# Kernel optimization log

Measured on AMD Instinct MI355X. Metric: run time of the kernel, lower is better.

## Reference

```python
import jax, jax.numpy as jnp
import numpy as np

NUM_HEADS = 8
D_MODEL = 512
D_K = D_MODEL // NUM_HEADS


def setup_inputs() -> dict:
    key = jax.random.key(0)
    ks = jax.random.split(key, 16)
    B, L, Dq = 4, 2048, 512
    s = 1.0 / np.sqrt(D_MODEL)
    inp = {
        "query": jax.random.normal(ks[0], (B, L, Dq), jnp.float32),
        "key": jax.random.normal(ks[1], (B, L, Dq), jnp.float32),
        "value": jax.random.normal(ks[2], (B, L, Dq), jnp.float32),
        "mask": jax.random.randint(ks[3], (B, L), 0, 2, jnp.int32),
        "Wq": jax.random.normal(ks[4], (Dq, D_MODEL), jnp.float32) * s,
        "bq": jax.random.normal(ks[5], (D_MODEL,), jnp.float32) * s,
        "Wk": jax.random.normal(ks[6], (Dq, D_MODEL), jnp.float32) * s,
        "bk": jax.random.normal(ks[7], (D_MODEL,), jnp.float32) * s,
        "Wv": jax.random.normal(ks[8], (Dq, D_MODEL), jnp.float32) * s,
        "bv": jax.random.normal(ks[9], (D_MODEL,), jnp.float32) * s,
        "Wo": jax.random.normal(ks[10], (D_MODEL, D_MODEL), jnp.float32) * s,
        "bo": jax.random.normal(ks[11], (D_MODEL,), jnp.float32) * s,
    }
    return inp


def _mha(query, key, value, mask, Wq, bq, Wk, bk, Wv, bv, Wo, bo):
    B, Q, _ = query.shape
    KV = key.shape[1]
    # projections, split into heads: (B, H, L, d_k)
    q = (query @ Wq + bq).reshape(B, Q, NUM_HEADS, D_K).transpose(0, 2, 1, 3)
    k = (key @ Wk + bk).reshape(B, KV, NUM_HEADS, D_K).transpose(0, 2, 1, 3)
    v = (value @ Wv + bv).reshape(B, KV, NUM_HEADS, D_K).transpose(0, 2, 1, 3)
    # full (B, H, Q, KV) score matrix, as in the original module
    scores = jnp.einsum("bhqd,bhkd->bhqk", q, k) / jnp.sqrt(jnp.asarray(D_K, q.dtype))
    m = (mask == 0)[:, None, None, :]  # (B,1,1,KV) broadcasting like unsqueeze(1)
    min_val = jnp.finfo(scores.dtype).min
    scores = jnp.where(m, min_val, scores)
    attn = jax.nn.softmax(scores, axis=-1)
    attn = jnp.where(m, 0.0, attn)
    xs = jnp.einsum("bhqk,bhkd->bhqd", attn, v)
    xs = xs.transpose(0, 2, 1, 3).reshape(B, Q, NUM_HEADS * D_K)
    return xs @ Wo + bo


def reference(query, key, value, mask, Wq, bq, Wk, bk, Wv, bv, Wo, bo):
    return _mha(query, key, value, mask, Wq, bq, Wk, bk, Wv, bv, Wo, bo)
```

## Files before the change

### kernel.cpp

```cpp
#include <hip/hip_runtime.h>
#include <math.h>

#define Bq 4
#define Lq 2048
#define NH 8
#define LDP6 36

typedef __attribute__((ext_vector_type(8))) __bf16 bf16x8;
typedef __attribute__((ext_vector_type(4))) float f32x4;
#define MFMA16(a,b,c) __builtin_amdgcn_mfma_f32_16x16x32_bf16(a,b,c,0,0,0)

__device__ __forceinline__ void async16(const void* g, void* l) {
    __builtin_amdgcn_global_load_lds(
        (const __attribute__((address_space(1))) unsigned int*)g,
        (__attribute__((address_space(3))) unsigned int*)l, 16, 0, 0);
}

__device__ __forceinline__ void splitbf(float x, ushort& h, ushort& l) {
    unsigned u = __float_as_uint(x);
    h = (ushort)(u >> 16);
    float hf = __uint_as_float(u & 0xffff0000u);
    l = (ushort)(__float_as_uint(x - hf) >> 16);
}
__device__ __forceinline__ ushort rnebf(float x) {
    unsigned u = __float_as_uint(x);
    return (ushort)((u + 0x7fffu + ((u >> 16) & 1u)) >> 16);
}

__global__ __launch_bounds__(256) void prep_kernel(
    const float* __restrict__ W0, const float* __restrict__ W1,
    const float* __restrict__ W2, const float* __restrict__ W3,
    ushort* __restrict__ WTh, ushort* __restrict__ WTl,
    const int* __restrict__ mask, int* __restrict__ idx, int* __restrict__ nvalid)
{
    const int tid = threadIdx.x;
    if (blockIdx.z == 4) {
        if (blockIdx.x >= 4 || blockIdx.y != 0) return;
        __shared__ int ss[256];
        const int b = blockIdx.x;
        int m[8], s = 0;
        #pragma unroll
        for (int j = 0; j < 8; ++j) { m[j] = (mask[b * 2048 + tid * 8 + j] != 0); s += m[j]; }
        int v = s;
        ss[tid] = v;
        __syncthreads();
        for (int off = 1; off < 256; off <<= 1) {
            int t_ = (tid >= off) ? ss[tid - off] : 0;
            __syncthreads();
            v += t_;
            ss[tid] = v;
            __syncthreads();
        }
        int pos = v - s;
        #pragma unroll
        for (int j = 0; j < 8; ++j) if (m[j]) idx[b * 2048 + pos++] = tid * 8 + j;
        int tot = ss[255];
        if (tid == 0) nvalid[b] = tot;
        for (int k = tot + tid; k < 2048; k += 256) idx[b * 2048 + k] = 0;
        return;
    }
    __shared__ float T[64][65];
    const int z = blockIdx.z;
    const float* W = (z == 0) ? W0 : (z == 1) ? W1 : (z == 2) ? W2 : W3;
    const int k0 = blockIdx.x * 64, n0 = blockIdx.y * 64;
    #pragma unroll
    for (int i = 0; i < 4; ++i) {
        int u = tid + i * 256;
        int row = u >> 4, c4 = (u & 15) * 4;
        float4 v = *(const float4*)(W + (size_t)(k0 + row) * 512 + n0 + c4);
        T[row][c4 + 0] = v.x; T[row][c4 + 1] = v.y; T[row][c4 + 2] = v.z; T[row][c4 + 3] = v.w;
    }
    __syncthreads();
    #pragma unroll
    for (int i = 0; i < 2; ++i) {
        int u = tid + i * 256;
        int d = u >> 3, c8 = (u & 7) * 8;
        ushort hs[8], ls[8];
        #pragma unroll
        for (int j = 0; j < 8; ++j) splitbf(T[c8 + j][d], hs[j], ls[j]);
        uint4 wh, wl;
        wh.x = hs[0] | ((unsigned)hs[1] << 16); wh.y = hs[2] | ((unsigned)hs[3] << 16);
        wh.z = hs[4] | ((unsigned)hs[5] << 16); wh.w = hs[6] | ((unsigned)hs[7] << 16);
        wl.x = ls[0] | ((unsigned)ls[1] << 16); wl.y = ls[2] | ((unsigned)ls[3] << 16);
        wl.z = ls[4] | ((unsigned)ls[5] << 16); wl.w = ls[6] | ((unsigned)ls[7] << 16);
        size_t off = (size_t)(z * 512 + n0 + d) * 512 + k0 + c8;
        *(uint4*)(WTh + off) = wh;
        *(uint4*)(WTl + off) = wl;
    }
}

union GS {
    struct {
        ushort A[2][4096];
        ushort Bh[2][4096];
        ushort Bl[2][4096];
    } s;
    ushort E[24576];
};

__global__ __launch_bounds__(256) void gemmqkv_kernel(
    const float* __restrict__ Xq, const float* __restrict__ Xk, const float* __restrict__ Xv,
    const int* __restrict__ idx, const int* __restrict__ nvalid,
    const ushort* __restrict__ BhT, const ushort* __restrict__ BlT,
    const float* __restrict__ b0, const float* __restrict__ b1, const float* __restrict__ b2,
    ushort* __restrict__ Qh, ushort* __restrict__ Khp, ushort* __restrict__ VhT)
{
    __shared__ __align__(16) GS gs;
    const int tid = threadIdx.x;
    const int wave = tid >> 6, lane = tid & 63;
    const int l15 = lane & 15, quad = lane >> 4;
    const int m0 = blockIdx.x * 128;
    const int yy = blockIdx.y;
    const int mi = yy >> 2, n0 = (yy & 3) * 128;
    const int nglob = mi * 512 + n0;
    const int b = m0 >> 11;

    if (mi >= 1) {
        int nv = nvalid[b];
        int nvpad = ((nv + 127) >> 7) << 7;
        if ((m0 & 2047) >= nvpad) return;
    }

    const float* X = (mi == 0) ? Xq : (mi == 1) ? Xk : Xv;
    const float* bias = (mi == 0) ? b0 : (mi == 1) ? b1 : b2;
    const int wm = (wave & 1) * 64, wn = (wave >> 1) * 64;

    const int am = tid >> 3, ak = (tid & 7) * 4;
    const float* asrc[4]; int adst[4];
    #pragma unroll
    for (int i = 0; i < 4; ++i) {
        int row = am + 32 * i;
        int grow = m0 + row, r = grow & 2047;
        int srow = (mi == 0) ? grow : (b * 2048 + idx[b * 2048 + r]);
        asrc[i] = X + (size_t)srow * 512 + ak;
        int c = (tid & 7) >> 1;
        int cp = c ^ ((row >> 1) & 3);
        adst[i] = row * 32 + cp * 8 + (tid & 1) * 4;
    }
    const int brow = lane >> 2;
    const int bcs = ((lane & 3) ^ (brow & 3)) * 8;
    const ushort* bsh[2]; const ushort* bsl[2]; int bdst[2];
    #pragma unroll
    for (int j = 0; j < 2; ++j) {
        int r2 = wave * 32 + j * 16 + brow;
        bsh[j] = BhT + (size_t)(nglob + r2) * 512 + bcs;
        bsl[j] = BlT + (size_t)(nglob + r2) * 512 + bcs;
        bdst[j] = wave * 1024 + j * 512 + lane * 8;
    }

    f32x4 acc[4][4];
    #pragma unroll
    for (int i = 0; i < 4; ++i)
        #pragma unroll
        for (int j = 0; j < 4; ++j) acc[i][j] = (f32x4){0.f, 0.f, 0.f, 0.f};

    float4 av[4];
    #pragma unroll
    for (int i = 0; i < 4; ++i) av[i] = *(const float4*)(asrc[i]);
    #pragma unroll
    for (int j = 0; j < 2; ++j) {
        async16(bsh[j], &gs.s.Bh[0][bdst[j]]);
        async16(bsl[j], &gs.s.Bl[0][bdst[j]]);
    }
    #pragma unroll
    for (int i = 0; i < 4; ++i) {
        ushort4 h4;
        h4.x = rnebf(av[i].x); h4.y = rnebf(av[i].y);
        h4.z = rnebf(av[i].z); h4.w = rnebf(av[i].w);
        *(ushort4*)&gs.s.A[0][adst[i]] = h4;
    }

    for (int t = 0; t < 16; ++t) {
        const int p = t & 1;
        __syncthreads();
        if (t < 15) {
            const int kn = (t + 1) * 32;
            #pragma unroll
            for (int j = 0; j < 2; ++j) {
                async16(bsh[j] + kn, &gs.s.Bh[1 - p][bdst[j]]);
                async16(bsl[j] + kn, &gs.s.Bl[1 - p][bdst[j]]);
            }
            #pragma unroll
            for (int i = 0; i < 4; ++i) av[i] = *(const float4*)(asrc[i] + kn);
        }
        bf16x8 af[4];
        #pragma unroll
        for (int ms = 0; ms < 4; ++ms) {
            int off = (wm + ms * 16 + l15) * 32 + (quad ^ ((l15 >> 1) & 3)) * 8;
            af[ms] = *(const bf16x8*)&gs.s.A[p][off];
        }
        #pragma unroll
        for (int ns = 0; ns < 4; ++ns) {
            int off = (wn + ns * 16 + l15) * 32 + (quad ^ (l15 & 3)) * 8;
            bf16x8 bfh = *(const bf16x8*)&gs.s.Bh[p][off];
            bf16x8 bfl = *(const bf16x8*)&gs.s.Bl[p][off];
            #pragma unroll
            for (int ms = 0; ms < 4; ++ms) {
                acc[ms][ns] = MFMA16(af[ms], bfl, acc[ms][ns]);
                acc[ms][ns] = MFMA16(af[ms], bfh, acc[ms][ns]);
            }
        }
        if (t < 15) {
            #pragma unroll
            for (int i = 0; i < 4; ++i) {
                ushort4 h4;
                h4.x = rnebf(av[i].x); h4.y = rnebf(av[i].y);
                h4.z = rnebf(av[i].z); h4.w = rnebf(av[i].w);
                *(ushort4*)&gs.s.A[1 - p][adst[i]] = h4;
            }
        }
    }

    #pragma unroll
    for (int ns = 0; ns < 4; ++ns) {
        float bv = bias[n0 + wn + ns * 16 + l15];
        #pragma unroll
        for (int ms = 0; ms < 4; ++ms)
            #pragma unroll
            for (int r = 0; r < 4; ++r) acc[ms][ns][r] += bv;
    }

    const int h0 = n0 >> 6;
    const int rr0 = m0 & 2047;
    __syncthreads();
    #pragma unroll
    for (int ms = 0; ms < 4; ++ms) {
        #pragma unroll
        for (int ns = 0; ns < 4; ++ns) {
            int cl = wn + ns * 16 + l15;
            int rl = wm + ms * 16 + quad * 4;
            if (mi == 2) {
                ushort4 w4;
                #pragma unroll
                for (int r = 0; r < 4; ++r) ((ushort*)&w4)[r] = rnebf(acc[ms][ns][r]);
                *(ushort4*)&gs.E[cl * 136 + rl] = w4;
            } else {
                #pragma unroll
                for (int r = 0; r < 4; ++r) gs.E[(rl + r) * 136 + cl] = rnebf(acc[ms][ns][r]);
            }
        }
    }
    __syncthreads();
    if (mi == 2) {
        #pragma unroll
        for (int i = 0; i < 8; ++i) {
            int idx2 = tid + i * 256;
            int d = idx2 >> 4, rg = idx2 & 15;
            int head = d >> 6, dd = d & 63;
            uint4 u = *(const uint4*)&gs.E[d * 136 + rg * 8];
            *(uint4*)&VhT[((size_t)(b * 8 + h0 + head) * 64 + dd) * 2048 + rr0 + rg * 8] = u;
        }
    } else {
        ushort* dst = (mi == 0) ? Qh : Khp;
        #pragma unroll
        for (int i = 0; i < 8; ++i) {
            int idx2 = tid + i * 256;
            int row = idx2 >> 4, cg = idx2 & 15;
            int head = cg >> 3, c8 = (cg & 7) * 8;
            uint4 u = *(const uint4*)&gs.E[row * 136 + cg * 8];
            *(uint4*)&dst[((size_t)(b * 8 + h0 + head) * 2048 + rr0 + row) * 64 + c8] = u;
        }
    }
}

__global__ __launch_bounds__(256) void gemmo_kernel(
    const ushort* __restrict__ Ap,
    const ushort* __restrict__ BhT, const ushort* __restrict__ BlT,
    const float* __restrict__ bias, float* __restrict__ Cf)
{
    __shared__ __align__(16) GS gs;
    const int tid = threadIdx.x;
    const int wave = tid >> 6, lane = tid & 63;
    const int l15 = lane & 15, quad = lane >> 4;
    const int m0 = blockIdx.x * 128;
    const int n0 = blockIdx.y * 128;
    const int wm = (wave & 1) * 64, wn = (wave >> 1) * 64;

    const int arow = lane >> 2;
    const int acs = ((lane & 3) ^ ((arow >> 1) & 3)) * 8;
    const ushort* asrc[2]; int adst[2];
    #pragma unroll
    for (int j = 0; j < 2; ++j) {
        int rb = wave * 2 + j;
        asrc[j] = Ap + (size_t)(m0 + rb * 16 + arow) * 512 + acs;
        adst[j] = rb * 512 + lane * 8;
    }
    const int brow = lane >> 2;
    const int bcs = ((lane & 3) ^ (brow & 3)) * 8;
    const ushort* bsh[2]; const ushort* bsl[2]; int bdst[2];
    #pragma unroll
    for (int j = 0; j < 2; ++j) {
        int r2 = wave * 32 + j * 16 + brow;
        bsh[j] = BhT + (size_t)(n0 + r2) * 512 + bcs;
        bsl[j] = BlT + (size_t)(n0 + r2) * 512 + bcs;
        bdst[j] = wave * 1024 + j * 512 + lane * 8;
    }

    f32x4 acc[4][4];
    #pragma unroll
    for (int i = 0; i < 4; ++i)
        #pragma unroll
        for (int j = 0; j < 4; ++j) acc[i][j] = (f32x4){0.f, 0.f, 0.f, 0.f};

    #pragma unroll
    for (int j = 0; j < 2; ++j) {
        async16(asrc[j], &gs.s.A[0][adst[j]]);
        async16(bsh[j], &gs.s.Bh[0][bdst[j]]);
        async16(bsl[j], &gs.s.Bl[0][bdst[j]]);
    }

    for (int t = 0; t < 16; ++t) {
        const int p = t & 1;
        __syncthreads();
        if (t < 15) {
            const int kn = (t + 1) * 32;
            #pragma unroll
            for (int j = 0; j < 2; ++j) {
                async16(asrc[j] + kn, &gs.s.A[1 - p][adst[j]]);
                async16(bsh[j] + kn, &gs.s.Bh[1 - p][bdst[j]]);
                async16(bsl[j] + kn, &gs.s.Bl[1 - p][bdst[j]]);
            }
        }
        bf16x8 af[4];
        #pragma unroll
        for (int ms = 0; ms < 4; ++ms) {
            int off = (wm + ms * 16 + l15) * 32 + (quad ^ ((l15 >> 1) & 3)) * 8;
            af[ms] = *(const bf16x8*)&gs.s.A[p][off];
        }
        #pragma unroll
        for (int ns = 0; ns < 4; ++ns) {
            int off = (wn + ns * 16 + l15) * 32 + (quad ^ (l15 & 3)) * 8;
            bf16x8 bfh = *(const bf16x8*)&gs.s.Bh[p][off];
            bf16x8 bfl = *(const bf16x8*)&gs.s.Bl[p][off];
            #pragma unroll
            for (int ms = 0; ms < 4; ++ms) {
                acc[ms][ns] = MFMA16(af[ms], bfl, acc[ms][ns]);
                acc[ms][ns] = MFMA16(af[ms], bfh, acc[ms][ns]);
            }
        }
    }

    #pragma unroll
    for (int ns = 0; ns < 4; ++ns) {
        float bv = bias[n0 + wn + ns * 16 + l15];
        #pragma unroll
        for (int ms = 0; ms < 4; ++ms) {
            int col = n0 + wn + ns * 16 + l15;
            #pragma unroll
            for (int r = 0; r < 4; ++r)
                Cf[(size_t)(m0 + wm + ms * 16 + quad * 4 + r) * 512 + col] = acc[ms][ns][r] + bv;
        }
    }
}

union SmemU {
    struct { ushort KVs[2][4][4096]; ushort Pp[8][64 * LDP6]; } p1;
    struct { float Obuf[4][64 * 68]; float Lbuf[4][64]; } p2;
};

__global__ __launch_bounds__(512, 2) void attn3_kernel(
    const ushort* __restrict__ Qh, const ushort* __restrict__ Kh,
    const ushort* __restrict__ VhT, const int* __restrict__ nvalid,
    ushort* __restrict__ XS)
{
    __shared__ SmemU smem;
    const int tid = threadIdx.x;
    const int wave = tid >> 6, lane = tid & 63;
    const int l15 = lane & 15, quad = lane >> 4;
    const int w4 = wave & 3, half = wave >> 2;
    const int bh = blockIdx.x, b = bh >> 3, h = bh & 7;
    const int q0 = blockIdx.y * 256;

    const int nv = nvalid[b];
    const int nt = (nv + 127) >> 7;
    const int kvofs = half * 64 * nt;

    bf16x8 qf[4][2];
    #pragma unroll
    for (int qs = 0; qs < 4; ++qs) {
        size_t qb = ((size_t)bh * 2048 + q0 + w4 * 64 + qs * 16 + l15) * 64 + quad * 8;
        qf[qs][0] = *(const bf16x8*)(Qh + qb);
        qf[qs][1] = *(const bf16x8*)(Qh + qb + 32);
    }

    const f32x4 z = {0.f, 0.f, 0.f, 0.f};
    f32x4 oacc[4][4];
    #pragma unroll
    for (int i = 0; i < 4; ++i)
        #pragma unroll
        for (int j = 0; j < 4; ++j) oacc[i][j] = z;
    float lacc[4] = {0.f, 0.f, 0.f, 0.f};

    const int rloc = lane >> 3, gsw = (lane & 7) ^ rloc;
    const ushort* sb[4]; size_t sstep[4]; int dofs[4];
    #pragma unroll
    for (int i = 0; i < 4; ++i) {
        int cc = wave * 4 + i;
        int hc = cc >> 4, r16 = cc & 15, pc = r16 >> 3, ic = r16 & 7;
        if (pc == 0) {
            sb[i] = Kh + ((size_t)(bh * 2048 + hc * 64 * nt + ic * 8 + rloc)) * 64 + gsw * 8;
            sstep[i] = (size_t)64 * 64;
        } else {
            sb[i] = VhT + ((size_t)(bh * 64 + ic * 8 + rloc)) * 2048 + hc * 64 * nt + gsw * 8;
            sstep[i] = 64;
        }
        dofs[i] = (hc * 2 + pc) * 4096 + ic * 512;
    }

    const int sw0 = (quad ^ (l15 & 7)) * 8;
    const float SCL = 0.18033688011112042f;

    if (nt > 0) {
        #pragma unroll
        for (int i = 0; i < 4; ++i)
            async16(sb[i], &smem.p1.KVs[0][0][0] + dofs[i]);
    }

    for (int t = 0; t < nt; ++t) {
        __syncthreads();
        if (t + 1 < nt) {
            #pragma unroll
            for (int i = 0; i < 4; ++i)
                async16(sb[i] + (size_t)(t + 1) * sstep[i], &smem.p1.KVs[(t + 1) & 1][0][0] + dofs[i]);
        }
        const int p = t & 1;
        const ushort* K0 = smem.p1.KVs[p][half * 2 + 0];
        const ushort* V0 = smem.p1.KVs[p][half * 2 + 1];
        ushort* Pw = smem.p1.Pp[wave];

        #pragma unroll
        for (int ks = 0; ks < 2; ++ks) {
            #pragma unroll
            for (int kt2 = 0; kt2 < 2; ++kt2) {
                const int kt = ks * 2 + kt2;
                const int kb = (kt * 16 + l15) * 64;
                bf16x8 ka0 = *(const bf16x8*)&K0[kb + sw0];
                bf16x8 ka1 = *(const bf16x8*)&K0[kb + (sw0 ^ 32)];
                const int kbase = kvofs + t * 64 + kt * 16 + quad * 4;
                float bias[4];
                #pragma unroll
                for (int r = 0; r < 4; ++r) bias[r] = (kbase + r < nv) ? 0.f : -1e38f;
                #pragma unroll
                for (int qs = 0; qs < 4; ++qs) {
                    f32x4 a = z;
                    a = MFMA16(ka0, qf[qs][0], a);
                    a = MFMA16(ka1, qf[qs][1], a);
                    float pv[4];
                    #pragma unroll
                    for (int r = 0; r < 4; ++r) {
                        float x = __builtin_fmaf(a[r], SCL, bias[r]);
                        float e; asm("v_exp_f32 %0, %1" : "=v"(e) : "v"(x));
                        lacc[qs] += e;
                        pv[r] = e;
                    }
                    unsigned u01, u23;
                    asm("v_cvt_pk_bf16_f32 %0, %1, %2" : "=v"(u01) : "v"(pv[0]), "v"(pv[1]));
                    asm("v_cvt_pk_bf16_f32 %0, %1, %2" : "=v"(u23) : "v"(pv[2]), "v"(pv[3]));
                    uint2 w2; w2.x = u01; w2.y = u23;
                    *(uint2*)&Pw[(qs * 16 + l15) * LDP6 + kt2 * 16 + quad * 4] = w2;
                }
            }
            const int svo = sw0 ^ (ks * 32);
            bf16x8 pf[4];
            #pragma unroll
            for (int qs = 0; qs < 4; ++qs)
                pf[qs] = *(const bf16x8*)&Pw[(qs * 16 + l15) * LDP6 + quad * 8];
            #pragma unroll
            for (int dsub = 0; dsub < 4; ++dsub) {
                const int vb = (dsub * 16 + l15) * 64;
                bf16x8 vh = *(const bf16x8*)&V0[vb + svo];
                #pragma unroll
                for (int qs = 0; qs < 4; ++qs)
                    oacc[qs][dsub] = MFMA16(vh, pf[qs], oacc[qs][dsub]);
            }
        }
    }

    float lv[4];
    #pragma unroll
    for (int qs = 0; qs < 4; ++qs) {
        float v = lacc[qs];
        v += __shfl_xor(v, 16);
        v += __shfl_xor(v, 32);
        lv[qs] = v;
    }

    __syncthreads();
    if (half == 1) {
        #pragma unroll
        for (int qs = 0; qs < 4; ++qs) {
            #pragma unroll
            for (int dsub = 0; dsub < 4; ++dsub) {
                float4 o4 = {oacc[qs][dsub][0], oacc[qs][dsub][1], oacc[qs][dsub][2], oacc[qs][dsub][3]};
                *(float4*)&smem.p2.Obuf[w4][(qs * 16 + l15) * 68 + dsub * 16 + quad * 4] = o4;
            }
            if (quad == 0) smem.p2.Lbuf[w4][qs * 16 + l15] = lv[qs];
        }
    }
    __syncthreads();
    if (half == 0) {
        #pragma unroll
        for (int qs = 0; qs < 4; ++qs) {
            float ltot = lv[qs] + smem.p2.Lbuf[w4][qs * 16 + l15];
            float inv = (ltot > 0.f) ? 1.f / ltot : 0.f;
            int row = q0 + w4 * 64 + qs * 16 + l15;
            ushort* rp = XS + ((size_t)(b * 2048 + row)) * 512 + h * 64;
            #pragma unroll
            for (int dsub = 0; dsub < 4; ++dsub) {
                float4 p4 = *(const float4*)&smem.p2.Obuf[w4][(qs * 16 + l15) * 68 + dsub * 16 + quad * 4];
                ushort4 hv;
                hv.x = rnebf((oacc[qs][dsub][0] + p4.x) * inv);
                hv.y = rnebf((oacc[qs][dsub][1] + p4.y) * inv);
                hv.z = rnebf((oacc[qs][dsub][2] + p4.z) * inv);
                hv.w = rnebf((oacc[qs][dsub][3] + p4.w) * inv);
                *(ushort4*)&rp[dsub * 16 + quad * 4] = hv;
            }
        }
    }
}

extern "C" void kernel_launch(void* const* d_in, const int* in_sizes, int n_in,
                              void* d_out, int out_size, void* d_ws, size_t ws_size,
                              hipStream_t stream) {
    const float* query = (const float*)d_in[0];
    const float* key   = (const float*)d_in[1];
    const float* value = (const float*)d_in[2];
    const int*   mask  = (const int*)d_in[3];
    const float* Wq = (const float*)d_in[4];
    const float* bq = (const float*)d_in[5];
    const float* Wk = (const float*)d_in[6];
    const float* bk = (const float*)d_in[7];
    const float* Wv = (const float*)d_in[8];
    const float* bv = (const float*)d_in[9];
    const float* Wo = (const float*)d_in[10];
    const float* bo = (const float*)d_in[11];

    char* w = (char*)d_ws;
    const size_t MB = (size_t)1 << 20;
    ushort* Qh  = (ushort*)(w + 0 * MB);
    ushort* XS  = (ushort*)(w + 8 * MB);
    ushort* Khp = (ushort*)(w + 16 * MB);
    ushort* VhT = (ushort*)(w + 24 * MB);
    ushort* WTh = (ushort*)(w + 32 * MB);
    ushort* WTl = (ushort*)(w + 34 * MB);
    int* idxbuf = (int*)(w + 36 * MB);
    int* nvbuf  = (int*)(w + 36 * MB + 65536);

    prep_kernel<<<dim3(8, 8, 5), 256, 0, stream>>>(
        Wq, Wk, Wv, Wo, WTh, WTl, mask, idxbuf, nvbuf);
    gemmqkv_kernel<<<dim3(64, 12), 256, 0, stream>>>(
        query, key, value, idxbuf, nvbuf, WTh, WTl, bq, bk, bv, Qh, Khp, VhT);
    attn3_kernel<<<dim3(32, 8), 512, 0, stream>>>(Qh, Khp, VhT, nvbuf, XS);
    gemmo_kernel<<<dim3(64, 4), 256, 0, stream>>>(
        XS, WTh + (size_t)1536 * 512, WTl + (size_t)1536 * 512, bo, (float*)d_out);
}
```

Baseline: 208.1 us.

## Pre-convert QKV inputs to bf16 and drop low-part weight MFMA

The prep kernel now also converts query/key/value from fp32 to bf16 into a workspace buffer. The QKV GEMM can then load A tiles with async global-to-LDS copies instead of register loads plus in-loop rounding. The QKV GEMM also drops the low-order bf16 weight correction term, halving its MFMA count and B-tile traffic. The cost is an extra full pass over the inputs in prep, lower accuracy from single-bf16 weights, and a grid with many early-exit blocks.

```diff
diff --git a/kernel.cpp b/kernel.cpp
--- a/kernel.cpp
+++ b/kernel.cpp
@@ -31,13 +31,62 @@
     const float* __restrict__ W0, const float* __restrict__ W1,
     const float* __restrict__ W2, const float* __restrict__ W3,
     ushort* __restrict__ WTh, ushort* __restrict__ WTl,
-    const int* __restrict__ mask, int* __restrict__ idx, int* __restrict__ nvalid)
+    const int* __restrict__ mask, int* __restrict__ idx, int* __restrict__ nvalid,
+    const float* __restrict__ X0, const float* __restrict__ X1, const float* __restrict__ X2,
+    ushort* __restrict__ Xr)
 {
     const int tid = threadIdx.x;
-    if (blockIdx.z == 4) {
-        if (blockIdx.x >= 4 || blockIdx.y != 0) return;
-        __shared__ int ss[256];
-        const int b = blockIdx.x;
+    const int z = blockIdx.z;
+    if (z < 3) {
+        const float* X = (z == 0) ? X0 : (z == 1) ? X1 : X2;
+        const size_t ebase = (size_t)blockIdx.x * 2048 + (size_t)tid * 8;
+        float4 a = *(const float4*)(X + ebase);
+        float4 bb = *(const float4*)(X + ebase + 4);
+        float vv[8] = {a.x, a.y, a.z, a.w, bb.x, bb.y, bb.z, bb.w};
+        ushort hs[8];
+        #pragma unroll
+        for (int j = 0; j < 8; ++j) hs[j] = rnebf(vv[j]);
+        uint4 wh;
+        wh.x = hs[0] | ((unsigned)hs[1] << 16); wh.y = hs[2] | ((unsigned)hs[3] << 16);
+        wh.z = hs[4] | ((unsigned)hs[5] << 16); wh.w = hs[6] | ((unsigned)hs[7] << 16);
+        *(uint4*)(Xr + (size_t)z * 8192 * 512 + ebase) = wh;
+        return;
+    }
+    const int x = blockIdx.x;
+    __shared__ float T[64][65];
+    __shared__ int ss[256];
+    if (x < 256) {
+        const int m = x >> 6;
+        const float* W = (m == 0) ? W0 : (m == 1) ? W1 : (m == 2) ? W2 : W3;
+        const int k0 = ((x >> 3) & 7) * 64, n0 = (x & 7) * 64;
+        #pragma unroll
+        for (int i = 0; i < 4; ++i) {
+            int u = tid + i * 256;
+            int row = u >> 4, c4 = (u & 15) * 4;
+            float4 v = *(const float4*)(W + (size_t)(k0 + row) * 512 + n0 + c4);
+            T[row][c4 + 0] = v.x; T[row][c4 + 1] = v.y; T[row][c4 + 2] = v.z; T[row][c4 + 3] = v.w;
+        }
+        __syncthreads();
+        #pragma unroll
+        for (int i = 0; i < 2; ++i) {
+            int u = tid + i * 256;
+            int d = u >> 3, c8 = (u & 7) * 8;
+            ushort hs[8], ls[8];
+            #pragma unroll
+            for (int j = 0; j < 8; ++j) splitbf(T[c8 + j][d], hs[j], ls[j]);
+            uint4 wh, wl;
+            wh.x = hs[0] | ((unsigned)hs[1] << 16); wh.y = hs[2] | ((unsigned)hs[3] << 16);
+            wh.z = hs[4] | ((unsigned)hs[5] << 16); wh.w = hs[6] | ((unsigned)hs[7] << 16);
+            wl.x = ls[0] | ((unsigned)ls[1] << 16); wl.y = ls[2] | ((unsigned)ls[3] << 16);
+            wl.z = ls[4] | ((unsigned)ls[5] << 16); wl.w = ls[6] | ((unsigned)ls[7] << 16);
+            size_t off = (size_t)(m * 512 + n0 + d) * 512 + k0 + c8;
+            *(uint4*)(WTh + off) = wh;
+            *(uint4*)(WTl + off) = wl;
+        }
+        return;
+    }
+    if (x < 260) {
+        const int b = x - 256;
         int m[8], s = 0;
         #pragma unroll
         for (int j = 0; j < 8; ++j) { m[j] = (mask[b * 2048 + tid * 8 + j] != 0); s += m[j]; }
@@ -57,51 +106,21 @@
         int tot = ss[255];
         if (tid == 0) nvalid[b] = tot;
         for (int k = tot + tid; k < 2048; k += 256) idx[b * 2048 + k] = 0;
-        return;
-    }
-    __shared__ float T[64][65];
-    const int z = blockIdx.z;
-    const float* W = (z == 0) ? W0 : (z == 1) ? W1 : (z == 2) ? W2 : W3;
-    const int k0 = blockIdx.x * 64, n0 = blockIdx.y * 64;
-    #pragma unroll
-    for (int i = 0; i < 4; ++i) {
-        int u = tid + i * 256;
-        int row = u >> 4, c4 = (u & 15) * 4;
-        float4 v = *(const float4*)(W + (size_t)(k0 + row) * 512 + n0 + c4);
-        T[row][c4 + 0] = v.x; T[row][c4 + 1] = v.y; T[row][c4 + 2] = v.z; T[row][c4 + 3] = v.w;
-    }
-    __syncthreads();
-    #pragma unroll
-    for (int i = 0; i < 2; ++i) {
-        int u = tid + i * 256;
-        int d = u >> 3, c8 = (u & 7) * 8;
-        ushort hs[8], ls[8];
-        #pragma unroll
-        for (int j = 0; j < 8; ++j) splitbf(T[c8 + j][d], hs[j], ls[j]);
-        uint4 wh, wl;
-        wh.x = hs[0] | ((unsigned)hs[1] << 16); wh.y = hs[2] | ((unsigned)hs[3] << 16);
-        wh.z = hs[4] | ((unsigned)hs[5] << 16); wh.w = hs[6] | ((unsigned)hs[7] << 16);
-        wl.x = ls[0] | ((unsigned)ls[1] << 16); wl.y = ls[2] | ((unsigned)ls[3] << 16);
-        wl.z = ls[4] | ((unsigned)ls[5] << 16); wl.w = ls[6] | ((unsigned)ls[7] << 16);
-        size_t off = (size_t)(z * 512 + n0 + d) * 512 + k0 + c8;
-        *(uint4*)(WTh + off) = wh;
-        *(uint4*)(WTl + off) = wl;
     }
 }
 
 union GS {
     struct {
         ushort A[2][4096];
-        ushort Bh[2][4096];
-        ushort Bl[2][4096];
+        ushort B[2][4096];
     } s;
-    ushort E[24576];
+    ushort E[17408];
 };
 
 __global__ __launch_bounds__(256) void gemmqkv_kernel(
-    const float* __restrict__ Xq, const float* __restrict__ Xk, const float* __restrict__ Xv,
+    const ushort* __restrict__ Xr,
     const int* __restrict__ idx, const int* __restrict__ nvalid,
-    const ushort* __restrict__ BhT, const ushort* __restrict__ BlT,
+    const ushort* __restrict__ BT,
     const float* __restrict__ b0, const float* __restrict__ b1, const float* __restrict__ b2,
     ushort* __restrict__ Qh, ushort* __restrict__ Khp, ushort* __restrict__ VhT)
 {
@@ -121,30 +140,29 @@
         if ((m0 & 2047) >= nvpad) return;
     }
 
-    const float* X = (mi == 0) ? Xq : (mi == 1) ? Xk : Xv;
     const float* bias = (mi == 0) ? b0 : (mi == 1) ? b1 : b2;
     const int wm = (wave & 1) * 64, wn = (wave >> 1) * 64;
 
-    const int am = tid >> 3, ak = (tid & 7) * 4;
-    const float* asrc[4]; int adst[4];
-    #pragma unroll
-    for (int i = 0; i < 4; ++i) {
-        int row = am + 32 * i;
+    const ushort* AZ = Xr + (size_t)mi * 8192 * 512;
+    const int arow = lane >> 2;
+    const int acs = ((lane & 3) ^ ((arow >> 1) & 3)) * 8;
+    const ushort* asrc[2]; int adst[2];
+    #pragma unroll
+    for (int j = 0; j < 2; ++j) {
+        int rb = wave * 2 + j;
+        int row = rb * 16 + arow;
         int grow = m0 + row, r = grow & 2047;
         int srow = (mi == 0) ? grow : (b * 2048 + idx[b * 2048 + r]);
-        asrc[i] = X + (size_t)srow * 512 + ak;
-        int c = (tid & 7) >> 1;
-        int cp = c ^ ((row >> 1) & 3);
-        adst[i] = row * 32 + cp * 8 + (tid & 1) * 4;
+        asrc[j] = AZ + (size_t)srow * 512 + acs;
+        adst[j] = rb * 512 + lane * 8;
     }
     const int brow = lane >> 2;
     const int bcs = ((lane & 3) ^ (brow & 3)) * 8;
-    const ushort* bsh[2]; const ushort* bsl[2]; int bdst[2];
+    const ushort* bsp[2]; int bdst[2];
     #pragma unroll
     for (int j = 0; j < 2; ++j) {
         int r2 = wave * 32 + j * 16 + brow;
-        bsh[j] = BhT + (size_t)(nglob + r2) * 512 + bcs;
-        bsl[j] = BlT + (size_t)(nglob + r2) * 512 + bcs;
+        bsp[j] = BT + (size_t)(nglob + r2) * 512 + bcs;
         bdst[j] = wave * 1024 + j * 512 + lane * 8;
     }
 
@@ -154,20 +172,10 @@
         #pragma unroll
         for (int j = 0; j < 4; ++j) acc[i][j] = (f32x4){0.f, 0.f, 0.f, 0.f};
 
-    float4 av[4];
-    #pragma unroll
-    for (int i = 0; i < 4; ++i) av[i] = *(const float4*)(asrc[i]);
     #pragma unroll
     for (int j = 0; j < 2; ++j) {
-        async16(bsh[j], &gs.s.Bh[0][bdst[j]]);
-        async16(bsl[j], &gs.s.Bl[0][bdst[j]]);
-    }
-    #pragma unroll
-    for (int i = 0; i < 4; ++i) {
-        ushort4 h4;
-        h4.x = rnebf(av[i].x); h4.y = rnebf(av[i].y);
-        h4.z = rnebf(av[i].z); h4.w = rnebf(av[i].w);
-        *(ushort4*)&gs.s.A[0][adst[i]] = h4;
+        async16(asrc[j], &gs.s.A[0][adst[j]]);
+        async16(bsp[j], &gs.s.B[0][bdst[j]]);
     }
 
     for (int t = 0; t < 16; ++t) {
@@ -177,11 +185,9 @@
             const int kn = (t + 1) * 32;
             #pragma unroll
             for (int j = 0; j < 2; ++j) {
-                async16(bsh[j] + kn, &gs.s.Bh[1 - p][bdst[j]]);
-                async16(bsl[j] + kn, &gs.s.Bl[1 - p][bdst[j]]);
-            }
-            #pragma unroll
-            for (int i = 0; i < 4; ++i) av[i] = *(const float4*)(asrc[i] + kn);
+                async16(asrc[j] + kn, &gs.s.A[1 - p][adst[j]]);
+                async16(bsp[j] + kn, &gs.s.B[1 - p][bdst[j]]);
+            }
         }
         bf16x8 af[4];
         #pragma unroll
@@ -192,22 +198,10 @@
         #pragma unroll
         for (int ns = 0; ns < 4; ++ns) {
             int off = (wn + ns * 16 + l15) * 32 + (quad ^ (l15 & 3)) * 8;
-            bf16x8 bfh = *(const bf16x8*)&gs.s.Bh[p][off];
-            bf16x8 bfl = *(const bf16x8*)&gs.s.Bl[p][off];
-            #pragma unroll
-            for (int ms = 0; ms < 4; ++ms) {
-                acc[ms][ns] = MFMA16(af[ms], bfl, acc[ms][ns]);
-                acc[ms][ns] = MFMA16(af[ms], bfh, acc[ms][ns]);
-            }
-        }
-        if (t < 15) {
-            #pragma unroll
-            for (int i = 0; i < 4; ++i) {
-                ushort4 h4;
-                h4.x = rnebf(av[i].x); h4.y = rnebf(av[i].y);
-                h4.z = rnebf(av[i].z); h4.w = rnebf(av[i].w);
-                *(ushort4*)&gs.s.A[1 - p][adst[i]] = h4;
-            }
+            bf16x8 bf = *(const bf16x8*)&gs.s.B[p][off];
+            #pragma unroll
+            for (int ms = 0; ms < 4; ++ms)
+                acc[ms][ns] = MFMA16(af[ms], bf, acc[ms][ns]);
         }
     }
 
@@ -263,12 +257,20 @@
     }
 }
 
+union GSO {
+    struct {
+        ushort A[2][4096];
+        ushort Bh[2][4096];
+        ushort Bl[2][4096];
+    } s;
+};
+
 __global__ __launch_bounds__(256) void gemmo_kernel(
     const ushort* __restrict__ Ap,
     const ushort* __restrict__ BhT, const ushort* __restrict__ BlT,
     const float* __restrict__ bias, float* __restrict__ Cf)
 {
-    __shared__ __align__(16) GS gs;
+    __shared__ __align__(16) GSO gs;
     const int tid = threadIdx.x;
     const int wave = tid >> 6, lane = tid & 63;
     const int l15 = lane & 15, quad = lane >> 4;
@@ -545,11 +547,12 @@
     ushort* WTl = (ushort*)(w + 34 * MB);
     int* idxbuf = (int*)(w + 36 * MB);
     int* nvbuf  = (int*)(w + 36 * MB + 65536);
-
-    prep_kernel<<<dim3(8, 8, 5), 256, 0, stream>>>(
-        Wq, Wk, Wv, Wo, WTh, WTl, mask, idxbuf, nvbuf);
+    ushort* Xr  = (ushort*)(w + 40 * MB);
+
+    prep_kernel<<<dim3(2048, 1, 4), 256, 0, stream>>>(
+        Wq, Wk, Wv, Wo, WTh, WTl, mask, idxbuf, nvbuf, query, key, value, Xr);
     gemmqkv_kernel<<<dim3(64, 12), 256, 0, stream>>>(
-        query, key, value, idxbuf, nvbuf, WTh, WTl, bq, bk, bv, Qh, Khp, VhT);
+        Xr, idxbuf, nvbuf, WTh, bq, bk, bv, Qh, Khp, VhT);
     attn3_kernel<<<dim3(32, 8), 512, 0, stream>>>(Qh, Khp, VhT, nvbuf, XS);
     gemmo_kernel<<<dim3(64, 4), 256, 0, stream>>>(
         XS, WTh + (size_t)1536 * 512, WTl + (size_t)1536 * 512, bo, (float*)d_out);
```

Measured after the change: 184.8 us. 1.13x faster.
